# Kernel tuning notes

Measured on AMD Instinct MI355X. Metric: run time of the kernel, lower is better.

## Reference

```python
import jax, jax.numpy as jnp
import numpy as np

B, XDIM, S = 32768, 32, 16
N_COMBINE = XDIM - 2  # 30 combines with out_channels=S (block0 + middle blocks)


def setup_inputs() -> dict:
    key = jax.random.key(0)
    k1, k2, k3, k4 = jax.random.split(key, 4)
    x = jax.random.randint(k1, (B, XDIM), 0, 2, dtype=jnp.int32)  # binary data
    leaf_logits = jax.random.normal(k2, (XDIM, S), dtype=jnp.float32)  # Bernoulli leaf logits per var
    sum_weights = jax.random.normal(k3, (N_COMBINE, S * S, S), dtype=jnp.float32)
    sum_weights_last = jax.random.normal(k4, (S * S, 1), dtype=jnp.float32)
    return {"x": x, "leaf_logits": leaf_logits, "sum_weights": sum_weights,
            "sum_weights_last": sum_weights_last}


def _combine(a, b, W):
    # a, b: [B, S] log-likelihoods; W: [S*S, OC] raw sum weights.
    # CrossProduct in log domain: out[:, i*S + j] = a[:, i] + b[:, j]
    cross = (a[:, :, None] + b[:, None, :]).reshape(a.shape[0], S * S)  # [B, S*S]
    logw = jax.nn.log_softmax(W, axis=0)  # normalize over in_channels
    # Sum node in log domain: logsumexp over input channels
    return jax.nn.logsumexp(cross[:, :, None] + logw[None, :, :], axis=1)  # [B, OC]


def reference(x, leaf_logits, sum_weights, sum_weights_last):
    xf = x.astype(jnp.float32)[:, :, None]  # [B, XDIM, 1]
    # Bernoulli leaf log-prob: x*log(sigmoid(l)) + (1-x)*log(1-sigmoid(l))
    lp = (xf * jax.nn.log_sigmoid(leaf_logits)[None]
          + (1.0 - xf) * jax.nn.log_sigmoid(-leaf_logits)[None])  # [B, XDIM, S]

    # block 0: combine leaves of vars 0 and 1
    curr = _combine(lp[:, 0], lp[:, 1], sum_weights[0])  # [B, S]

    # middle blocks: fold in vars 2 .. XDIM-2
    mid_leaves = jnp.swapaxes(lp[:, 2:XDIM - 1], 0, 1)  # [XDIM-3, B, S]

    def step(c, inp):
        leaf, W = inp
        return _combine(c, leaf, W), None

    curr, _ = jax.lax.scan(step, curr, (mid_leaves, sum_weights[1:]))

    # final block: fold in last var with out_channels=1 root sum
    out = _combine(curr, lp[:, XDIM - 1], sum_weights_last)  # [B, 1]
    return out[:, None, :]  # [B, 1, 1] to match torch output shape
```

## Files before the change

### kernel.cpp

```cpp
#include <hip/hip_runtime.h>

using uint = unsigned int;

#define DW_LO    0
#define DW_HIb   7616
#define DW_FT    15232
#define DW_DELTA 15360
#define DW_BASE  15392
#define DW_EB0   15396
#define DW_TOT   15616
#define WFW      16384
#define WLW      31744

template<int K>
__device__ __forceinline__ int roti(int x) {
    return __builtin_amdgcn_update_dpp(0, x, 0x120 | K, 0xF, 0xF, true);
}
template<int K>
__device__ __forceinline__ float rotf(float x) {
    return __builtin_bit_cast(float, roti<K>(__builtin_bit_cast(int, x)));
}
__device__ __forceinline__ float rowmax16(float d) {
    d = fmaxf(d, rotf<1>(d)); d = fmaxf(d, rotf<2>(d));
    d = fmaxf(d, rotf<4>(d)); d = fmaxf(d, rotf<8>(d));
    return d;
}
__device__ __forceinline__ float rowsum16(float d) {
    d += rotf<1>(d); d += rotf<2>(d); d += rotf<4>(d); d += rotf<8>(d);
    return d;
}
__device__ __forceinline__ float logsig(float z) {
    return fminf(z, 0.f) - log1pf(__expf(-fabsf(z)));
}
__device__ __forceinline__ uint bfpack(float a, float b) {
    uint ua = __builtin_bit_cast(uint, a);
    uint ub = __builtin_bit_cast(uint, b);
    ua = (ua + 0x7fffu + ((ua >> 16) & 1u)) >> 16;
    ub = ((ub + 0x7fffu + ((ub >> 16) & 1u)) >> 16) << 16;
    return ua | ub;
}
__device__ __forceinline__ float blo(uint u) { return __builtin_bit_cast(float, u << 16); }
__device__ __forceinline__ float bhi(uint u) { return __builtin_bit_cast(float, u & 0xffff0000u); }
__device__ __forceinline__ unsigned spread16(unsigned u) {
    u = (u | (u << 8)) & 0x00FF00FFu;
    u = (u | (u << 4)) & 0x0F0F0F0Fu;
    u = (u | (u << 2)) & 0x33333333u;
    u = (u | (u << 1)) & 0x55555555u;
    return u;
}

__global__ __launch_bounds__(256) void prep1(const float* __restrict__ sw,
                                             const float* __restrict__ swl,
                                             const float* __restrict__ ll,
                                             float* __restrict__ ws) {
    __shared__ float pm[256];
    __shared__ float ebs[32];
    __shared__ float BMs[64];
    const int tid = threadIdx.x;
    const int c = blockIdx.x;
    const int i = tid >> 4, oc = tid & 15;

    if (c < 30) {
        if (tid < 32) {
            int bb = tid >> 4;
            float l = ll[(c + 1) * 16 + oc];
            float lp = bb ? logsig(l) : logsig(-l);
            ebs[tid] = __expf(lp - rowmax16(lp));
        }
        const float* Wb = sw + c * 4096;
        float w[16]; float m = -1e30f;
        #pragma unroll
        for (int j = 0; j < 16; ++j) {
            w[j] = Wb[i * 256 + j * 16 + oc];
            m = fmaxf(m, w[j]);
        }
        pm[i * 16 + oc] = m;
        __syncthreads();
        float cm = pm[oc];
        #pragma unroll
        for (int r = 1; r < 16; ++r) cm = fmaxf(cm, pm[r * 16 + oc]);
        float e[16]; float s = 0.f;
        #pragma unroll
        for (int j = 0; j < 16; ++j) { e[j] = __expf(w[j] - cm); s += e[j]; }
        __syncthreads();
        pm[i * 16 + oc] = s;
        __syncthreads();
        float ss = pm[oc];
        #pragma unroll
        for (int r = 1; r < 16; ++r) ss += pm[r * 16 + oc];
        float inv = 1.0f / ss;
        float a0 = 0.f, a1 = 0.f;
        #pragma unroll
        for (int j = 0; j < 16; ++j) { a0 += ebs[j] * e[j]; a1 += ebs[16 + j] * e[j]; }
        ws[WFW + ((c * 2 + 0) * 16 + i) * 16 + oc] = a0 * inv;
        ws[WFW + ((c * 2 + 1) * 16 + i) * 16 + oc] = a1 * inv;
    } else {
        float v = swl[tid];
        float m = v;
        #pragma unroll
        for (int off = 32; off >= 1; off >>= 1) m = fmaxf(m, __shfl_xor(m, off));
        if ((tid & 63) == 0) pm[tid >> 6] = m;
        if (tid < 32) {
            int bb = tid >> 4;
            float l = ll[31 * 16 + oc];
            float lp = bb ? logsig(l) : logsig(-l);
            ebs[tid] = __expf(lp - rowmax16(lp));
        }
        __syncthreads();
        m = fmaxf(fmaxf(pm[0], pm[1]), fmaxf(pm[2], pm[3]));
        float e = __expf(v - m);
        float s = e;
        #pragma unroll
        for (int off = 32; off >= 1; off >>= 1) s += __shfl_xor(s, off);
        __syncthreads();
        if ((tid & 63) == 0) pm[tid >> 6] = s;
        __syncthreads();
        float inv = 1.0f / (pm[0] + pm[1] + pm[2] + pm[3]);
        float t0 = rowsum16(ebs[oc] * e);
        float t1 = rowsum16(ebs[16 + oc] * e);
        if (oc == 0) {
            ws[WLW + 0 + i]  = t0 * inv;
            ws[WLW + 16 + i] = t1 * inv;
        }
        if (tid < 64) {
            int var = tid >> 1, bb = tid & 1;
            float mm_ = -1e30f;
            #pragma unroll
            for (int j = 0; j < 16; ++j) {
                float l = ll[var * 16 + j];
                mm_ = fmaxf(mm_, bb ? logsig(l) : logsig(-l));
            }
            BMs[tid] = mm_;
        }
        if (tid >= 64 && tid < 96) {
            int u = tid - 64, bb = u >> 4, j = u & 15;
            float mm_ = -1e30f;
            #pragma unroll
            for (int jj = 0; jj < 16; ++jj) {
                float l = ll[jj];
                mm_ = fmaxf(mm_, bb ? logsig(l) : logsig(-l));
            }
            float l = ll[j];
            ws[DW_EB0 + u] = __expf((bb ? logsig(l) : logsig(-l)) - mm_);
        }
        __syncthreads();
        if (tid < 32) ws[DW_DELTA + tid] = BMs[2 * tid + 1] - BMs[2 * tid];
        if (tid < 64) {
            float vb = (tid < 32) ? BMs[2 * tid] : 0.f;
            #pragma unroll
            for (int off = 32; off >= 1; off >>= 1) vb += __shfl_xor(vb, off);
            if (tid == 0) ws[DW_BASE] = vb;
        }
    }
}

__global__ __launch_bounds__(256) void prep2(float* __restrict__ ws) {
    __shared__ __align__(16) float WFs[2048];
    __shared__ float Ts[1024];
    __shared__ float Ms[4096];
    const int tid = threadIdx.x;
    const int p = blockIdx.x;
    const int i = tid >> 4, oc = tid & 15;

    int s1 = roti<1>(oc) & 15,   s2 = roti<2>(oc) & 15,   s3 = roti<3>(oc) & 15;
    int s4 = roti<4>(oc) & 15,   s5 = roti<5>(oc) & 15,   s6 = roti<6>(oc) & 15;
    int s7 = roti<7>(oc) & 15,   s8 = roti<8>(oc) & 15,   s9 = roti<9>(oc) & 15;
    int s10 = roti<10>(oc) & 15, s11 = roti<11>(oc) & 15, s12 = roti<12>(oc) & 15;
    int s13 = roti<13>(oc) & 15, s14 = roti<14>(oc) & 15, s15 = roti<15>(oc) & 15;
    int sidx[16] = {oc, s1, s2, s3, s4, s5, s6, s7, s8, s9, s10, s11, s12, s13, s14, s15};

    if (p < 7) {
        const float4* src = (const float4*)(ws + WFW + p * 2048);
        ((float4*)WFs)[tid]       = src[tid];
        ((float4*)WFs)[256 + tid] = src[256 + tid];
        __syncthreads();

        float wf0[2], wf2[2];
        wf0[0] = WFs[0 * 256 + i * 16 + oc];
        wf0[1] = WFs[1 * 256 + i * 16 + oc];
        wf2[0] = WFs[4 * 256 + i * 16 + oc];
        wf2[1] = WFs[5 * 256 + i * 16 + oc];

        float t1[4], t2[4];
        {
            float w10 = WFs[2 * 256 + oc * 16 + oc], w11 = WFs[3 * 256 + oc * 16 + oc];
            float w30 = WFs[6 * 256 + oc * 16 + oc], w31 = WFs[7 * 256 + oc * 16 + oc];
            t1[0] = wf0[0] * w10; t1[1] = wf0[1] * w10;
            t1[2] = wf0[0] * w11; t1[3] = wf0[1] * w11;
            t2[0] = wf2[0] * w30; t2[1] = wf2[1] * w30;
            t2[2] = wf2[0] * w31; t2[3] = wf2[1] * w31;
        }
        #define QSTEP(T) { \
            float r0 = rotf<T>(wf0[0]), r1 = rotf<T>(wf0[1]); \
            float w10 = WFs[2 * 256 + sidx[T] * 16 + oc], w11 = WFs[3 * 256 + sidx[T] * 16 + oc]; \
            t1[0] = fmaf(r0, w10, t1[0]); t1[1] = fmaf(r1, w10, t1[1]); \
            t1[2] = fmaf(r0, w11, t1[2]); t1[3] = fmaf(r1, w11, t1[3]); \
            float q0 = rotf<T>(wf2[0]), q1 = rotf<T>(wf2[1]); \
            float w30 = WFs[6 * 256 + sidx[T] * 16 + oc], w31 = WFs[7 * 256 + sidx[T] * 16 + oc]; \
            t2[0] = fmaf(q0, w30, t2[0]); t2[1] = fmaf(q1, w30, t2[1]); \
            t2[2] = fmaf(q0, w31, t2[2]); t2[3] = fmaf(q1, w31, t2[3]); }
        QSTEP(1) QSTEP(2) QSTEP(3) QSTEP(4) QSTEP(5) QSTEP(6) QSTEP(7) QSTEP(8)
        QSTEP(9) QSTEP(10) QSTEP(11) QSTEP(12) QSTEP(13) QSTEP(14) QSTEP(15)
        #undef QSTEP

        #pragma unroll
        for (int b = 0; b < 4; ++b) Ts[b * 256 + i * 16 + oc] = t2[b];
        __syncthreads();

        float M[16];
        {
            float c0 = Ts[0 * 256 + oc * 16 + oc], c1 = Ts[1 * 256 + oc * 16 + oc];
            float c2 = Ts[2 * 256 + oc * 16 + oc], c3 = Ts[3 * 256 + oc * 16 + oc];
            #pragma unroll
            for (int b12 = 0; b12 < 4; ++b12) {
                M[b12 + 0]  = t1[b12] * c0;
                M[b12 + 4]  = t1[b12] * c1;
                M[b12 + 8]  = t1[b12] * c2;
                M[b12 + 12] = t1[b12] * c3;
            }
        }
        #define MSTEP(T) { \
            float c0 = Ts[0 * 256 + sidx[T] * 16 + oc], c1 = Ts[1 * 256 + sidx[T] * 16 + oc]; \
            float c2 = Ts[2 * 256 + sidx[T] * 16 + oc], c3 = Ts[3 * 256 + sidx[T] * 16 + oc]; \
            float r0 = rotf<T>(t1[0]), r1 = rotf<T>(t1[1]), r2 = rotf<T>(t1[2]), r3 = rotf<T>(t1[3]); \
            M[0]  = fmaf(r0, c0, M[0]);  M[1]  = fmaf(r1, c0, M[1]); \
            M[2]  = fmaf(r2, c0, M[2]);  M[3]  = fmaf(r3, c0, M[3]); \
            M[4]  = fmaf(r0, c1, M[4]);  M[5]  = fmaf(r1, c1, M[5]); \
            M[6]  = fmaf(r2, c1, M[6]);  M[7]  = fmaf(r3, c1, M[7]); \
            M[8]  = fmaf(r0, c2, M[8]);  M[9]  = fmaf(r1, c2, M[9]); \
            M[10] = fmaf(r2, c2, M[10]); M[11] = fmaf(r3, c2, M[11]); \
            M[12] = fmaf(r0, c3, M[12]); M[13] = fmaf(r1, c3, M[13]); \
            M[14] = fmaf(r2, c3, M[14]); M[15] = fmaf(r3, c3, M[15]); }
        MSTEP(1) MSTEP(2) MSTEP(3) MSTEP(4) MSTEP(5) MSTEP(6) MSTEP(7) MSTEP(8)
        MSTEP(9) MSTEP(10) MSTEP(11) MSTEP(12) MSTEP(13) MSTEP(14) MSTEP(15)
        #undef MSTEP

        #pragma unroll
        for (int v = 0; v < 16; ++v) Ms[v * 256 + i * 16 + oc] = M[v];
        __syncthreads();

        {
            int v = i, ocx = oc;
            const float* m = Ms + v * 256;
            float x0 = m[ocx * 16 + ocx];
            float x1 = m[s1 * 16 + ocx],   x2 = m[s2 * 16 + ocx],   x3 = m[s3 * 16 + ocx];
            float x4 = m[s4 * 16 + ocx],   x5 = m[s5 * 16 + ocx],   x6 = m[s6 * 16 + ocx];
            float x7 = m[s7 * 16 + ocx],   x8 = m[s8 * 16 + ocx],   x9 = m[s9 * 16 + ocx];
            float x10 = m[s10 * 16 + ocx], x11 = m[s11 * 16 + ocx], x12 = m[s12 * 16 + ocx];
            float x13 = m[s13 * 16 + ocx], x14 = m[s14 * 16 + ocx], x15 = m[s15 * 16 + ocx];
            uint4 lo4, hi4;
            lo4.x = bfpack(x0, x1);   lo4.y = bfpack(x2, x3);
            lo4.z = bfpack(x4, x5);   lo4.w = bfpack(x6, x7);
            hi4.x = bfpack(x8, x9);   hi4.y = bfpack(x10, x11);
            hi4.z = bfpack(x12, x13); hi4.w = bfpack(x14, x15);
            uint* wsu = (uint*)ws;
            int dw = p * 1088 + v * 68 + ocx * 4;
            *(uint4*)(wsu + dw) = lo4;
            *(uint4*)(wsu + DW_HIb + dw) = hi4;
        }
    } else {
        const float4* src = (const float4*)(ws + WFW + 28 * 512);
        ((float4*)WFs)[tid] = src[tid];
        __syncthreads();

        float wf28[2];
        wf28[0] = WFs[0 * 256 + i * 16 + oc];
        wf28[1] = WFs[1 * 256 + i * 16 + oc];
        float t01[4];
        {
            float w0 = WFs[2 * 256 + oc * 16 + oc], w1 = WFs[3 * 256 + oc * 16 + oc];
            t01[0] = wf28[0] * w0; t01[1] = wf28[1] * w0;
            t01[2] = wf28[0] * w1; t01[3] = wf28[1] * w1;
        }
        #define FSTEP(T) { \
            float r0 = rotf<T>(wf28[0]), r1 = rotf<T>(wf28[1]); \
            float w0 = WFs[2 * 256 + sidx[T] * 16 + oc], w1 = WFs[3 * 256 + sidx[T] * 16 + oc]; \
            t01[0] = fmaf(r0, w0, t01[0]); t01[1] = fmaf(r1, w0, t01[1]); \
            t01[2] = fmaf(r0, w1, t01[2]); t01[3] = fmaf(r1, w1, t01[3]); }
        FSTEP(1) FSTEP(2) FSTEP(3) FSTEP(4) FSTEP(5) FSTEP(6) FSTEP(7) FSTEP(8)
        FSTEP(9) FSTEP(10) FSTEP(11) FSTEP(12) FSTEP(13) FSTEP(14) FSTEP(15)
        #undef FSTEP

        float wl0 = ws[WLW + oc], wl1 = ws[WLW + 16 + oc];
        #pragma unroll
        for (int v = 0; v < 8; ++v) {
            float f = rowsum16(t01[v & 3] * ((v >> 2) ? wl1 : wl0));
            if (oc == 0) ws[DW_FT + v * 16 + i] = f;
        }
    }
}

__device__ __forceinline__ float quadstep(const uint* sPT, float acc, int dw) {
    uint4 wl4 = *(const uint4*)(sPT + dw);
    uint4 wh4 = *(const uint4*)(sPT + DW_HIb + dw);
    float d0 = acc * blo(wl4.x);
    d0 = fmaf(rotf<1>(acc), bhi(wl4.x), d0);
    d0 = fmaf(rotf<2>(acc), blo(wl4.y), d0);
    d0 = fmaf(rotf<3>(acc), bhi(wl4.y), d0);
    d0 = fmaf(rotf<4>(acc), blo(wl4.z), d0);
    d0 = fmaf(rotf<5>(acc), bhi(wl4.z), d0);
    d0 = fmaf(rotf<6>(acc), blo(wl4.w), d0);
    d0 = fmaf(rotf<7>(acc), bhi(wl4.w), d0);
    float d1 = rotf<8>(acc) * blo(wh4.x);
    d1 = fmaf(rotf<9>(acc),  bhi(wh4.x), d1);
    d1 = fmaf(rotf<10>(acc), blo(wh4.y), d1);
    d1 = fmaf(rotf<11>(acc), bhi(wh4.y), d1);
    d1 = fmaf(rotf<12>(acc), blo(wh4.z), d1);
    d1 = fmaf(rotf<13>(acc), bhi(wh4.z), d1);
    d1 = fmaf(rotf<14>(acc), blo(wh4.w), d1);
    d1 = fmaf(rotf<15>(acc), bhi(wh4.w), d1);
    return d0 + d1;
}

__global__ __launch_bounds__(512, 4) void spn_main(const int* __restrict__ x,
                                                   const float* __restrict__ ws,
                                                   float* __restrict__ out) {
    __shared__ __align__(16) float sL[DW_TOT];
    const int tid = threadIdx.x;
    const int g = tid >> 4, oc = tid & 15;
    const int b0 = blockIdx.x * 64 + g;
    const int b1 = b0 + 32;

    int2 xa = *(const int2*)(x + b0 * 32 + 2 * oc);
    int2 xb = *(const int2*)(x + b1 * 32 + 2 * oc);
    unsigned long long ma0 = __ballot(xa.x & 1);
    unsigned long long ma1 = __ballot(xa.y & 1);
    unsigned long long mb0 = __ballot(xb.x & 1);
    unsigned long long mb1 = __ballot(xb.y & 1);
    const int gw = g & 3;
    unsigned bitsA = spread16((unsigned)(ma0 >> (gw * 16)) & 0xffffu)
                   | (spread16((unsigned)(ma1 >> (gw * 16)) & 0xffffu) << 1);
    unsigned bitsB = spread16((unsigned)(mb0 >> (gw * 16)) & 0xffffu)
                   | (spread16((unsigned)(mb1 >> (gw * 16)) & 0xffffu) << 1);

    for (int k = tid; k < DW_TOT / 4; k += 512)
        ((float4*)sL)[k] = ((const float4*)ws)[k];
    __syncthreads();

    float2 dl = *(const float2*)(sL + DW_DELTA + 2 * oc);
    float pa = ((xa.x & 1) ? dl.x : 0.f) + ((xa.y & 1) ? dl.y : 0.f);
    float pb = ((xb.x & 1) ? dl.x : 0.f) + ((xb.y & 1) ? dl.y : 0.f);
    float base = sL[DW_BASE];
    float LA = base + rowsum16(pa);
    float LB = base + rowsum16(pb);

    float accA = sL[DW_EB0 + (bitsA & 1) * 16 + oc];
    float accB = sL[DW_EB0 + (bitsB & 1) * 16 + oc];
    const uint* sPT = (const uint*)sL;
    const int ocd = oc * 4;

    #pragma unroll
    for (int p = 0; p < 7; ++p) {
        int dwA = p * 1088 + (int)((bitsA >> (4 * p + 1)) & 15) * 68 + ocd;
        int dwB = p * 1088 + (int)((bitsB >> (4 * p + 1)) & 15) * 68 + ocd;
        float dA = quadstep(sPT, accA, dwA);
        float dB = quadstep(sPT, accB, dwB);
        if (p & 1) {
            float mA = rowmax16(dA), mB = rowmax16(dB);
            accA = dA * __builtin_amdgcn_rcpf(mA);
            accB = dB * __builtin_amdgcn_rcpf(mB);
            LA += __logf(mA);
            LB += __logf(mB);
        } else {
            accA = dA; accB = dB;
        }
    }

    float tsA = rowsum16(accA * sL[DW_FT + ((bitsA >> 29) & 7) * 16 + oc]);
    float tsB = rowsum16(accB * sL[DW_FT + ((bitsB >> 29) & 7) * 16 + oc]);
    if (oc == 0) {
        out[b0] = LA + __logf(tsA);
        out[b1] = LB + __logf(tsB);
    }
}

extern "C" void kernel_launch(void* const* d_in, const int* in_sizes, int n_in,
                              void* d_out, int out_size, void* d_ws, size_t ws_size,
                              hipStream_t stream) {
    const int*   x   = (const int*)d_in[0];
    const float* ll  = (const float*)d_in[1];
    const float* sw  = (const float*)d_in[2];
    const float* swl = (const float*)d_in[3];
    float* out = (float*)d_out;
    float* ws  = (float*)d_ws;

    hipLaunchKernelGGL(prep1,    dim3(31),  dim3(256), 0, stream, sw, swl, ll, ws);
    hipLaunchKernelGGL(prep2,    dim3(8),   dim3(256), 0, stream, ws);
    hipLaunchKernelGGL(spn_main, dim3(512), dim3(512), 0, stream, x, ws, out);
}
```

Baseline: 24.83 us.

## Fuse the two weight-preparation kernels into one eight-block prep kernel

Merges prep1 (per-combine softmax of weights folded with leaf probabilities) and prep2 (products of pairs of combine matrices packed into bf16 tables) into a single kernel. Each 512-thread block now computes the softmax for its own four combine matrices in shared memory, then runs the matrix products directly. The WFW/WLW global round trip goes away, along with one kernel launch and the dependency gap between launches. In exchange, only 8 blocks now do the softmax work that 31 blocks did before, and half the threads sit idle during the product phase, which lengthens the serial critical path inside prep.

```diff
diff --git a/kernel.cpp b/kernel.cpp
--- a/kernel.cpp
+++ b/kernel.cpp
@@ -9,8 +9,6 @@
 #define DW_BASE  15392
 #define DW_EB0   15396
 #define DW_TOT   15616
-#define WFW      16384
-#define WLW      31744
 
 template<int K>
 __device__ __forceinline__ int roti(int x) {
@@ -49,118 +47,25 @@
     return u;
 }
 
-__global__ __launch_bounds__(256) void prep1(const float* __restrict__ sw,
-                                             const float* __restrict__ swl,
-                                             const float* __restrict__ ll,
-                                             float* __restrict__ ws) {
-    __shared__ float pm[256];
-    __shared__ float ebs[32];
-    __shared__ float BMs[64];
-    const int tid = threadIdx.x;
-    const int c = blockIdx.x;
-    const int i = tid >> 4, oc = tid & 15;
-
-    if (c < 30) {
-        if (tid < 32) {
-            int bb = tid >> 4;
-            float l = ll[(c + 1) * 16 + oc];
-            float lp = bb ? logsig(l) : logsig(-l);
-            ebs[tid] = __expf(lp - rowmax16(lp));
-        }
-        const float* Wb = sw + c * 4096;
-        float w[16]; float m = -1e30f;
-        #pragma unroll
-        for (int j = 0; j < 16; ++j) {
-            w[j] = Wb[i * 256 + j * 16 + oc];
-            m = fmaxf(m, w[j]);
-        }
-        pm[i * 16 + oc] = m;
-        __syncthreads();
-        float cm = pm[oc];
-        #pragma unroll
-        for (int r = 1; r < 16; ++r) cm = fmaxf(cm, pm[r * 16 + oc]);
-        float e[16]; float s = 0.f;
-        #pragma unroll
-        for (int j = 0; j < 16; ++j) { e[j] = __expf(w[j] - cm); s += e[j]; }
-        __syncthreads();
-        pm[i * 16 + oc] = s;
-        __syncthreads();
-        float ss = pm[oc];
-        #pragma unroll
-        for (int r = 1; r < 16; ++r) ss += pm[r * 16 + oc];
-        float inv = 1.0f / ss;
-        float a0 = 0.f, a1 = 0.f;
-        #pragma unroll
-        for (int j = 0; j < 16; ++j) { a0 += ebs[j] * e[j]; a1 += ebs[16 + j] * e[j]; }
-        ws[WFW + ((c * 2 + 0) * 16 + i) * 16 + oc] = a0 * inv;
-        ws[WFW + ((c * 2 + 1) * 16 + i) * 16 + oc] = a1 * inv;
-    } else {
-        float v = swl[tid];
-        float m = v;
-        #pragma unroll
-        for (int off = 32; off >= 1; off >>= 1) m = fmaxf(m, __shfl_xor(m, off));
-        if ((tid & 63) == 0) pm[tid >> 6] = m;
-        if (tid < 32) {
-            int bb = tid >> 4;
-            float l = ll[31 * 16 + oc];
-            float lp = bb ? logsig(l) : logsig(-l);
-            ebs[tid] = __expf(lp - rowmax16(lp));
-        }
-        __syncthreads();
-        m = fmaxf(fmaxf(pm[0], pm[1]), fmaxf(pm[2], pm[3]));
-        float e = __expf(v - m);
-        float s = e;
-        #pragma unroll
-        for (int off = 32; off >= 1; off >>= 1) s += __shfl_xor(s, off);
-        __syncthreads();
-        if ((tid & 63) == 0) pm[tid >> 6] = s;
-        __syncthreads();
-        float inv = 1.0f / (pm[0] + pm[1] + pm[2] + pm[3]);
-        float t0 = rowsum16(ebs[oc] * e);
-        float t1 = rowsum16(ebs[16 + oc] * e);
-        if (oc == 0) {
-            ws[WLW + 0 + i]  = t0 * inv;
-            ws[WLW + 16 + i] = t1 * inv;
-        }
-        if (tid < 64) {
-            int var = tid >> 1, bb = tid & 1;
-            float mm_ = -1e30f;
-            #pragma unroll
-            for (int j = 0; j < 16; ++j) {
-                float l = ll[var * 16 + j];
-                mm_ = fmaxf(mm_, bb ? logsig(l) : logsig(-l));
-            }
-            BMs[tid] = mm_;
-        }
-        if (tid >= 64 && tid < 96) {
-            int u = tid - 64, bb = u >> 4, j = u & 15;
-            float mm_ = -1e30f;
-            #pragma unroll
-            for (int jj = 0; jj < 16; ++jj) {
-                float l = ll[jj];
-                mm_ = fmaxf(mm_, bb ? logsig(l) : logsig(-l));
-            }
-            float l = ll[j];
-            ws[DW_EB0 + u] = __expf((bb ? logsig(l) : logsig(-l)) - mm_);
-        }
-        __syncthreads();
-        if (tid < 32) ws[DW_DELTA + tid] = BMs[2 * tid + 1] - BMs[2 * tid];
-        if (tid < 64) {
-            float vb = (tid < 32) ? BMs[2 * tid] : 0.f;
-            #pragma unroll
-            for (int off = 32; off >= 1; off >>= 1) vb += __shfl_xor(vb, off);
-            if (tid == 0) ws[DW_BASE] = vb;
-        }
-    }
-}
-
-__global__ __launch_bounds__(256) void prep2(float* __restrict__ ws) {
+__global__ __launch_bounds__(512) void prep(const float* __restrict__ sw,
+                                            const float* __restrict__ swl,
+                                            const float* __restrict__ ll,
+                                            float* __restrict__ ws) {
     __shared__ __align__(16) float WFs[2048];
+    __shared__ float pm[1024];
+    __shared__ float CM[64], CS[64];
+    __shared__ float ebs[128];
     __shared__ float Ts[1024];
     __shared__ float Ms[4096];
+    __shared__ float BMs[64];
+    __shared__ float WLs[32];
+    __shared__ float pml[16], psl[16];
+    __shared__ float CMl, CSl;
+
     const int tid = threadIdx.x;
     const int p = blockIdx.x;
-    const int i = tid >> 4, oc = tid & 15;
+    const int oc = tid & 15;
+    const int i0 = (tid >> 4) & 15;
 
     int s1 = roti<1>(oc) & 15,   s2 = roti<2>(oc) & 15,   s3 = roti<3>(oc) & 15;
     int s4 = roti<4>(oc) & 15,   s5 = roti<5>(oc) & 15,   s6 = roti<6>(oc) & 15;
@@ -170,77 +75,134 @@
     int sidx[16] = {oc, s1, s2, s3, s4, s5, s6, s7, s8, s9, s10, s11, s12, s13, s14, s15};
 
     if (p < 7) {
-        const float4* src = (const float4*)(ws + WFW + p * 2048);
-        ((float4*)WFs)[tid]       = src[tid];
-        ((float4*)WFs)[256 + tid] = src[256 + tid];
-        __syncthreads();
-
-        float wf0[2], wf2[2];
-        wf0[0] = WFs[0 * 256 + i * 16 + oc];
-        wf0[1] = WFs[1 * 256 + i * 16 + oc];
-        wf2[0] = WFs[4 * 256 + i * 16 + oc];
-        wf2[1] = WFs[5 * 256 + i * 16 + oc];
+        if (tid < 128) {
+            int cc = tid >> 5, bb = (tid >> 4) & 1, var = 4 * p + 1 + cc;
+            float l = ll[var * 16 + oc];
+            float lp = bb ? logsig(l) : logsig(-l);
+            ebs[tid] = __expf(lp - rowmax16(lp));
+        }
+        const float* Wb = sw + p * 4 * 4096;
+        const int cc0 = tid >> 8, cc1 = cc0 + 2;
+        float w0[16], w1[16];
+        float m0 = -1e30f, m1 = -1e30f;
+        #pragma unroll
+        for (int j = 0; j < 16; ++j) {
+            w0[j] = Wb[cc0 * 4096 + (i0 * 16 + j) * 16 + oc];
+            w1[j] = Wb[cc1 * 4096 + (i0 * 16 + j) * 16 + oc];
+            m0 = fmaxf(m0, w0[j]); m1 = fmaxf(m1, w1[j]);
+        }
+        pm[cc0 * 256 + oc * 16 + i0] = m0;
+        pm[cc1 * 256 + oc * 16 + i0] = m1;
+        __syncthreads();
+        if (tid < 64) {
+            const float* q = pm + (tid >> 4) * 256 + (tid & 15) * 16;
+            float m = q[0];
+            #pragma unroll
+            for (int r = 1; r < 16; ++r) m = fmaxf(m, q[r]);
+            CM[tid] = m;
+        }
+        __syncthreads();
+        float cm0 = CM[cc0 * 16 + oc], cm1 = CM[cc1 * 16 + oc];
+        float e0[16], e1[16];
+        float su0 = 0.f, su1 = 0.f;
+        #pragma unroll
+        for (int j = 0; j < 16; ++j) {
+            e0[j] = __expf(w0[j] - cm0); su0 += e0[j];
+            e1[j] = __expf(w1[j] - cm1); su1 += e1[j];
+        }
+        pm[cc0 * 256 + oc * 16 + i0] = su0;
+        pm[cc1 * 256 + oc * 16 + i0] = su1;
+        __syncthreads();
+        if (tid < 64) {
+            const float* q = pm + (tid >> 4) * 256 + (tid & 15) * 16;
+            float s = 0.f;
+            #pragma unroll
+            for (int r = 0; r < 16; ++r) s += q[r];
+            CS[tid] = 1.0f / s;
+        }
+        __syncthreads();
+        {
+            float inv0 = CS[cc0 * 16 + oc], inv1 = CS[cc1 * 16 + oc];
+            float a00 = 0.f, a01 = 0.f, a10 = 0.f, a11 = 0.f;
+            #pragma unroll
+            for (int j = 0; j < 16; ++j) {
+                a00 += ebs[(cc0 * 2 + 0) * 16 + j] * e0[j];
+                a01 += ebs[(cc0 * 2 + 1) * 16 + j] * e0[j];
+                a10 += ebs[(cc1 * 2 + 0) * 16 + j] * e1[j];
+                a11 += ebs[(cc1 * 2 + 1) * 16 + j] * e1[j];
+            }
+            WFs[(cc0 * 2 + 0) * 256 + i0 * 16 + oc] = a00 * inv0;
+            WFs[(cc0 * 2 + 1) * 256 + i0 * 16 + oc] = a01 * inv0;
+            WFs[(cc1 * 2 + 0) * 256 + i0 * 16 + oc] = a10 * inv1;
+            WFs[(cc1 * 2 + 1) * 256 + i0 * 16 + oc] = a11 * inv1;
+        }
+        __syncthreads();
 
         float t1[4], t2[4];
-        {
-            float w10 = WFs[2 * 256 + oc * 16 + oc], w11 = WFs[3 * 256 + oc * 16 + oc];
-            float w30 = WFs[6 * 256 + oc * 16 + oc], w31 = WFs[7 * 256 + oc * 16 + oc];
-            t1[0] = wf0[0] * w10; t1[1] = wf0[1] * w10;
-            t1[2] = wf0[0] * w11; t1[3] = wf0[1] * w11;
-            t2[0] = wf2[0] * w30; t2[1] = wf2[1] * w30;
-            t2[2] = wf2[0] * w31; t2[3] = wf2[1] * w31;
-        }
-        #define QSTEP(T) { \
-            float r0 = rotf<T>(wf0[0]), r1 = rotf<T>(wf0[1]); \
-            float w10 = WFs[2 * 256 + sidx[T] * 16 + oc], w11 = WFs[3 * 256 + sidx[T] * 16 + oc]; \
-            t1[0] = fmaf(r0, w10, t1[0]); t1[1] = fmaf(r1, w10, t1[1]); \
-            t1[2] = fmaf(r0, w11, t1[2]); t1[3] = fmaf(r1, w11, t1[3]); \
-            float q0 = rotf<T>(wf2[0]), q1 = rotf<T>(wf2[1]); \
-            float w30 = WFs[6 * 256 + sidx[T] * 16 + oc], w31 = WFs[7 * 256 + sidx[T] * 16 + oc]; \
-            t2[0] = fmaf(q0, w30, t2[0]); t2[1] = fmaf(q1, w30, t2[1]); \
-            t2[2] = fmaf(q0, w31, t2[2]); t2[3] = fmaf(q1, w31, t2[3]); }
-        QSTEP(1) QSTEP(2) QSTEP(3) QSTEP(4) QSTEP(5) QSTEP(6) QSTEP(7) QSTEP(8)
-        QSTEP(9) QSTEP(10) QSTEP(11) QSTEP(12) QSTEP(13) QSTEP(14) QSTEP(15)
-        #undef QSTEP
-
-        #pragma unroll
-        for (int b = 0; b < 4; ++b) Ts[b * 256 + i * 16 + oc] = t2[b];
-        __syncthreads();
-
-        float M[16];
-        {
-            float c0 = Ts[0 * 256 + oc * 16 + oc], c1 = Ts[1 * 256 + oc * 16 + oc];
-            float c2 = Ts[2 * 256 + oc * 16 + oc], c3 = Ts[3 * 256 + oc * 16 + oc];
-            #pragma unroll
-            for (int b12 = 0; b12 < 4; ++b12) {
-                M[b12 + 0]  = t1[b12] * c0;
-                M[b12 + 4]  = t1[b12] * c1;
-                M[b12 + 8]  = t1[b12] * c2;
-                M[b12 + 12] = t1[b12] * c3;
-            }
-        }
-        #define MSTEP(T) { \
-            float c0 = Ts[0 * 256 + sidx[T] * 16 + oc], c1 = Ts[1 * 256 + sidx[T] * 16 + oc]; \
-            float c2 = Ts[2 * 256 + sidx[T] * 16 + oc], c3 = Ts[3 * 256 + sidx[T] * 16 + oc]; \
-            float r0 = rotf<T>(t1[0]), r1 = rotf<T>(t1[1]), r2 = rotf<T>(t1[2]), r3 = rotf<T>(t1[3]); \
-            M[0]  = fmaf(r0, c0, M[0]);  M[1]  = fmaf(r1, c0, M[1]); \
-            M[2]  = fmaf(r2, c0, M[2]);  M[3]  = fmaf(r3, c0, M[3]); \
-            M[4]  = fmaf(r0, c1, M[4]);  M[5]  = fmaf(r1, c1, M[5]); \
-            M[6]  = fmaf(r2, c1, M[6]);  M[7]  = fmaf(r3, c1, M[7]); \
-            M[8]  = fmaf(r0, c2, M[8]);  M[9]  = fmaf(r1, c2, M[9]); \
-            M[10] = fmaf(r2, c2, M[10]); M[11] = fmaf(r3, c2, M[11]); \
-            M[12] = fmaf(r0, c3, M[12]); M[13] = fmaf(r1, c3, M[13]); \
-            M[14] = fmaf(r2, c3, M[14]); M[15] = fmaf(r3, c3, M[15]); }
-        MSTEP(1) MSTEP(2) MSTEP(3) MSTEP(4) MSTEP(5) MSTEP(6) MSTEP(7) MSTEP(8)
-        MSTEP(9) MSTEP(10) MSTEP(11) MSTEP(12) MSTEP(13) MSTEP(14) MSTEP(15)
-        #undef MSTEP
-
-        #pragma unroll
-        for (int v = 0; v < 16; ++v) Ms[v * 256 + i * 16 + oc] = M[v];
-        __syncthreads();
-
-        {
-            int v = i, ocx = oc;
+        if (tid < 256) {
+            float wf0[2], wf2[2];
+            wf0[0] = WFs[0 * 256 + i0 * 16 + oc];
+            wf0[1] = WFs[1 * 256 + i0 * 16 + oc];
+            wf2[0] = WFs[4 * 256 + i0 * 16 + oc];
+            wf2[1] = WFs[5 * 256 + i0 * 16 + oc];
+            {
+                float w10 = WFs[2 * 256 + oc * 16 + oc], w11 = WFs[3 * 256 + oc * 16 + oc];
+                float w30 = WFs[6 * 256 + oc * 16 + oc], w31 = WFs[7 * 256 + oc * 16 + oc];
+                t1[0] = wf0[0] * w10; t1[1] = wf0[1] * w10;
+                t1[2] = wf0[0] * w11; t1[3] = wf0[1] * w11;
+                t2[0] = wf2[0] * w30; t2[1] = wf2[1] * w30;
+                t2[2] = wf2[0] * w31; t2[3] = wf2[1] * w31;
+            }
+            #define QSTEP(T) { \
+                float r0 = rotf<T>(wf0[0]), r1 = rotf<T>(wf0[1]); \
+                float w10 = WFs[2 * 256 + sidx[T] * 16 + oc], w11 = WFs[3 * 256 + sidx[T] * 16 + oc]; \
+                t1[0] = fmaf(r0, w10, t1[0]); t1[1] = fmaf(r1, w10, t1[1]); \
+                t1[2] = fmaf(r0, w11, t1[2]); t1[3] = fmaf(r1, w11, t1[3]); \
+                float q0 = rotf<T>(wf2[0]), q1 = rotf<T>(wf2[1]); \
+                float w30 = WFs[6 * 256 + sidx[T] * 16 + oc], w31 = WFs[7 * 256 + sidx[T] * 16 + oc]; \
+                t2[0] = fmaf(q0, w30, t2[0]); t2[1] = fmaf(q1, w30, t2[1]); \
+                t2[2] = fmaf(q0, w31, t2[2]); t2[3] = fmaf(q1, w31, t2[3]); }
+            QSTEP(1) QSTEP(2) QSTEP(3) QSTEP(4) QSTEP(5) QSTEP(6) QSTEP(7) QSTEP(8)
+            QSTEP(9) QSTEP(10) QSTEP(11) QSTEP(12) QSTEP(13) QSTEP(14) QSTEP(15)
+            #undef QSTEP
+            #pragma unroll
+            for (int b = 0; b < 4; ++b) Ts[b * 256 + i0 * 16 + oc] = t2[b];
+        }
+        __syncthreads();
+        if (tid < 256) {
+            float M[16];
+            {
+                float c0 = Ts[0 * 256 + oc * 16 + oc], c1 = Ts[1 * 256 + oc * 16 + oc];
+                float c2 = Ts[2 * 256 + oc * 16 + oc], c3 = Ts[3 * 256 + oc * 16 + oc];
+                #pragma unroll
+                for (int b12 = 0; b12 < 4; ++b12) {
+                    M[b12 + 0]  = t1[b12] * c0;
+                    M[b12 + 4]  = t1[b12] * c1;
+                    M[b12 + 8]  = t1[b12] * c2;
+                    M[b12 + 12] = t1[b12] * c3;
+                }
+            }
+            #define MSTEP(T) { \
+                float c0 = Ts[0 * 256 + sidx[T] * 16 + oc], c1 = Ts[1 * 256 + sidx[T] * 16 + oc]; \
+                float c2 = Ts[2 * 256 + sidx[T] * 16 + oc], c3 = Ts[3 * 256 + sidx[T] * 16 + oc]; \
+                float r0 = rotf<T>(t1[0]), r1 = rotf<T>(t1[1]), r2 = rotf<T>(t1[2]), r3 = rotf<T>(t1[3]); \
+                M[0]  = fmaf(r0, c0, M[0]);  M[1]  = fmaf(r1, c0, M[1]); \
+                M[2]  = fmaf(r2, c0, M[2]);  M[3]  = fmaf(r3, c0, M[3]); \
+                M[4]  = fmaf(r0, c1, M[4]);  M[5]  = fmaf(r1, c1, M[5]); \
+                M[6]  = fmaf(r2, c1, M[6]);  M[7]  = fmaf(r3, c1, M[7]); \
+                M[8]  = fmaf(r0, c2, M[8]);  M[9]  = fmaf(r1, c2, M[9]); \
+                M[10] = fmaf(r2, c2, M[10]); M[11] = fmaf(r3, c2, M[11]); \
+                M[12] = fmaf(r0, c3, M[12]); M[13] = fmaf(r1, c3, M[13]); \
+                M[14] = fmaf(r2, c3, M[14]); M[15] = fmaf(r3, c3, M[15]); }
+            MSTEP(1) MSTEP(2) MSTEP(3) MSTEP(4) MSTEP(5) MSTEP(6) MSTEP(7) MSTEP(8)
+            MSTEP(9) MSTEP(10) MSTEP(11) MSTEP(12) MSTEP(13) MSTEP(14) MSTEP(15)
+            #undef MSTEP
+            #pragma unroll
+            for (int v = 0; v < 16; ++v) Ms[v * 256 + i0 * 16 + oc] = M[v];
+        }
+        __syncthreads();
+        if (tid < 256) {
+            int v = i0, ocx = oc;
             const float* m = Ms + v * 256;
             float x0 = m[ocx * 16 + ocx];
             float x1 = m[s1 * 16 + ocx],   x2 = m[s2 * 16 + ocx],   x3 = m[s3 * 16 + ocx];
@@ -259,33 +221,140 @@
             *(uint4*)(wsu + DW_HIb + dw) = hi4;
         }
     } else {
-        const float4* src = (const float4*)(ws + WFW + 28 * 512);
-        ((float4*)WFs)[tid] = src[tid];
-        __syncthreads();
-
-        float wf28[2];
-        wf28[0] = WFs[0 * 256 + i * 16 + oc];
-        wf28[1] = WFs[1 * 256 + i * 16 + oc];
-        float t01[4];
+        if (tid < 96) {
+            int cb = tid >> 4, bb = cb & 1;
+            int var = (cb < 4) ? (29 + (cb >> 1)) : 31;
+            float l = ll[var * 16 + oc];
+            float lp = bb ? logsig(l) : logsig(-l);
+            ebs[tid] = __expf(lp - rowmax16(lp));
+        }
+        const int cc = tid >> 8;
+        float w[16]; float m0 = -1e30f;
+        #pragma unroll
+        for (int j = 0; j < 16; ++j) {
+            w[j] = sw[(28 + cc) * 4096 + (i0 * 16 + j) * 16 + oc];
+            m0 = fmaxf(m0, w[j]);
+        }
+        pm[cc * 256 + oc * 16 + i0] = m0;
+        float vL = 0.f;
+        if (tid >= 256) {
+            int u = tid - 256;
+            vL = swl[u];
+            float pmx = rowmax16(vL);
+            if ((u & 15) == 0) pml[u >> 4] = pmx;
+        }
+        __syncthreads();
+        if (tid < 32) {
+            const float* q = pm + (tid >> 4) * 256 + (tid & 15) * 16;
+            float m = q[0];
+            #pragma unroll
+            for (int r = 1; r < 16; ++r) m = fmaxf(m, q[r]);
+            CM[tid] = m;
+        }
+        if (tid == 256) {
+            float m = pml[0];
+            #pragma unroll
+            for (int r = 1; r < 16; ++r) m = fmaxf(m, pml[r]);
+            CMl = m;
+        }
+        __syncthreads();
+        float cm = CM[cc * 16 + oc];
+        float e[16]; float su = 0.f;
+        #pragma unroll
+        for (int j = 0; j < 16; ++j) { e[j] = __expf(w[j] - cm); su += e[j]; }
+        pm[cc * 256 + oc * 16 + i0] = su;
+        float eL = 0.f;
+        if (tid >= 256) {
+            int u = tid - 256;
+            eL = __expf(vL - CMl);
+            float ps = rowsum16(eL);
+            if ((u & 15) == 0) psl[u >> 4] = ps;
+        }
+        __syncthreads();
+        if (tid < 32) {
+            const float* q = pm + (tid >> 4) * 256 + (tid & 15) * 16;
+            float s = 0.f;
+            #pragma unroll
+            for (int r = 0; r < 16; ++r) s += q[r];
+            CS[tid] = 1.0f / s;
+        }
+        if (tid == 256) {
+            float s = 0.f;
+            #pragma unroll
+            for (int r = 0; r < 16; ++r) s += psl[r];
+            CSl = 1.0f / s;
+        }
+        __syncthreads();
         {
-            float w0 = WFs[2 * 256 + oc * 16 + oc], w1 = WFs[3 * 256 + oc * 16 + oc];
-            t01[0] = wf28[0] * w0; t01[1] = wf28[1] * w0;
-            t01[2] = wf28[0] * w1; t01[3] = wf28[1] * w1;
-        }
-        #define FSTEP(T) { \
-            float r0 = rotf<T>(wf28[0]), r1 = rotf<T>(wf28[1]); \
-            float w0 = WFs[2 * 256 + sidx[T] * 16 + oc], w1 = WFs[3 * 256 + sidx[T] * 16 + oc]; \
-            t01[0] = fmaf(r0, w0, t01[0]); t01[1] = fmaf(r1, w0, t01[1]); \
-            t01[2] = fmaf(r0, w1, t01[2]); t01[3] = fmaf(r1, w1, t01[3]); }
-        FSTEP(1) FSTEP(2) FSTEP(3) FSTEP(4) FSTEP(5) FSTEP(6) FSTEP(7) FSTEP(8)
-        FSTEP(9) FSTEP(10) FSTEP(11) FSTEP(12) FSTEP(13) FSTEP(14) FSTEP(15)
-        #undef FSTEP
-
-        float wl0 = ws[WLW + oc], wl1 = ws[WLW + 16 + oc];
-        #pragma unroll
-        for (int v = 0; v < 8; ++v) {
-            float f = rowsum16(t01[v & 3] * ((v >> 2) ? wl1 : wl0));
-            if (oc == 0) ws[DW_FT + v * 16 + i] = f;
+            float inv = CS[cc * 16 + oc];
+            float a0 = 0.f, a1 = 0.f;
+            #pragma unroll
+            for (int j = 0; j < 16; ++j) {
+                a0 += ebs[(cc * 2 + 0) * 16 + j] * e[j];
+                a1 += ebs[(cc * 2 + 1) * 16 + j] * e[j];
+            }
+            WFs[(cc * 2 + 0) * 256 + i0 * 16 + oc] = a0 * inv;
+            WFs[(cc * 2 + 1) * 256 + i0 * 16 + oc] = a1 * inv;
+        }
+        if (tid >= 256) {
+            int u = tid - 256, iw = u >> 4;
+            float t0 = rowsum16(ebs[64 + oc] * eL);
+            float t1 = rowsum16(ebs[80 + oc] * eL);
+            if (oc == 0) { WLs[iw] = t0 * CSl; WLs[16 + iw] = t1 * CSl; }
+        }
+        if (tid < 64) {
+            int var = tid >> 1, bb = tid & 1;
+            float mm_ = -1e30f;
+            #pragma unroll
+            for (int j = 0; j < 16; ++j) {
+                float l = ll[var * 16 + j];
+                mm_ = fmaxf(mm_, bb ? logsig(l) : logsig(-l));
+            }
+            BMs[tid] = mm_;
+        }
+        if (tid >= 64 && tid < 96) {
+            int u = tid - 64, bb = u >> 4, j = u & 15;
+            float mm_ = -1e30f;
+            #pragma unroll
+            for (int jj = 0; jj < 16; ++jj) {
+                float l = ll[jj];
+                mm_ = fmaxf(mm_, bb ? logsig(l) : logsig(-l));
+            }
+            float l = ll[j];
+            ws[DW_EB0 + u] = __expf((bb ? logsig(l) : logsig(-l)) - mm_);
+        }
+        __syncthreads();
+        if (tid < 256) {
+            float wf28[2];
+            wf28[0] = WFs[0 * 256 + i0 * 16 + oc];
+            wf28[1] = WFs[1 * 256 + i0 * 16 + oc];
+            float t01[4];
+            {
+                float w0_ = WFs[2 * 256 + oc * 16 + oc], w1_ = WFs[3 * 256 + oc * 16 + oc];
+                t01[0] = wf28[0] * w0_; t01[1] = wf28[1] * w0_;
+                t01[2] = wf28[0] * w1_; t01[3] = wf28[1] * w1_;
+            }
+            #define FSTEP(T) { \
+                float r0 = rotf<T>(wf28[0]), r1 = rotf<T>(wf28[1]); \
+                float w0_ = WFs[2 * 256 + sidx[T] * 16 + oc], w1_ = WFs[3 * 256 + sidx[T] * 16 + oc]; \
+                t01[0] = fmaf(r0, w0_, t01[0]); t01[1] = fmaf(r1, w0_, t01[1]); \
+                t01[2] = fmaf(r0, w1_, t01[2]); t01[3] = fmaf(r1, w1_, t01[3]); }
+            FSTEP(1) FSTEP(2) FSTEP(3) FSTEP(4) FSTEP(5) FSTEP(6) FSTEP(7) FSTEP(8)
+            FSTEP(9) FSTEP(10) FSTEP(11) FSTEP(12) FSTEP(13) FSTEP(14) FSTEP(15)
+            #undef FSTEP
+            float wl0 = WLs[oc], wl1 = WLs[16 + oc];
+            #pragma unroll
+            for (int v = 0; v < 8; ++v) {
+                float f = rowsum16(t01[v & 3] * ((v >> 2) ? wl1 : wl0));
+                if (oc == 0) ws[DW_FT + v * 16 + i0] = f;
+            }
+        }
+        if (tid < 32) ws[DW_DELTA + tid] = BMs[2 * tid + 1] - BMs[2 * tid];
+        if (tid < 64) {
+            float vb = (tid < 32) ? BMs[2 * tid] : 0.f;
+            #pragma unroll
+            for (int off = 32; off >= 1; off >>= 1) vb += __shfl_xor(vb, off);
+            if (tid == 0) ws[DW_BASE] = vb;
         }
     }
 }
@@ -384,7 +453,6 @@
     float* out = (float*)d_out;
     float* ws  = (float*)d_ws;
 
-    hipLaunchKernelGGL(prep1,    dim3(31),  dim3(256), 0, stream, sw, swl, ll, ws);
-    hipLaunchKernelGGL(prep2,    dim3(8),   dim3(256), 0, stream, ws);
+    hipLaunchKernelGGL(prep,     dim3(8),   dim3(512), 0, stream, sw, swl, ll, ws);
     hipLaunchKernelGGL(spn_main, dim3(512), dim3(512), 0, stream, x, ws, out);
 }
```

New measurement: 22.24 us (median of 2 runs). 10.5% less time.
